# Optimization experiments

Measured on AMD Instinct MI355X. Metric: run time of the kernel, lower is better.

Reference implementation:

```python
import jax, jax.numpy as jnp
import numpy as np

# Directable[TL_table[i]] for i = 0..7: (dx, dy) with dx=horizontal shift, dy=vertical shift
# dx=+1 -> shift right (zero-fill col 0), dx=-1 -> shift left; dy=+1 -> shift down, dy=-1 -> shift up.
DIRS = [(1, 1), (0, 1), (-1, 1), (1, 0), (-1, 0), (1, -1), (0, -1), (-1, -1)]


def _shift(img, dx, dy):
    # img: [B, H, W]; zero-padded shift equivalent to bmm with the sparse translation matrices
    if dx == 1:
        img = jnp.pad(img[..., :-1], ((0, 0), (0, 0), (1, 0)))
    elif dx == -1:
        img = jnp.pad(img[..., 1:], ((0, 0), (0, 0), (0, 1)))
    if dy == 1:
        img = jnp.pad(img[:, :-1, :], ((0, 0), (1, 0), (0, 0)))
    elif dy == -1:
        img = jnp.pad(img[:, 1:, :], ((0, 0), (0, 1), (0, 0)))
    return img


def _bce(p, t):
    # torch F.binary_cross_entropy clamps log terms at -100
    logp = jnp.maximum(jnp.log(p), -100.0)
    log1mp = jnp.maximum(jnp.log(1.0 - p), -100.0)
    return -jnp.mean(t * logp + (1.0 - t) * log1mp)


def setup_inputs() -> dict:
    key = jax.random.key(0)
    k1, k2, k3 = jax.random.split(key, 3)
    B, C, H, W = 16, 8, 512, 512
    c_map = jax.random.normal(k1, (B, C, H, W), dtype=jnp.float32)
    target = jax.random.randint(k2, (B, 1, H, W), 0, 2, dtype=jnp.int32)
    con_target = jax.random.randint(k3, (B, C, H, W), 0, 2, dtype=jnp.int32)
    return {"c_map": c_map, "target": target, "con_target": con_target}


def reference(c_map, target, con_target):
    target = target.astype(jnp.float32)        # [B,1,H,W]
    con_target = con_target.astype(jnp.float32)  # [B,8,H,W]

    p = jax.nn.sigmoid(c_map)  # [B,8,H,W]

    # Bilateral voting: shifted[i] = shift(p[:, 7-i]) in direction DIRS[i]
    shifted = jnp.stack(
        [_shift(p[:, 7 - i], dx, dy) for i, (dx, dy) in enumerate(DIRS)], axis=1
    )  # [B,8,H,W]
    vote_out = p * shifted                       # [B,8,H,W] (== bimap.squeeze(1))
    final_pred = jnp.max(vote_out, axis=1, keepdims=True)  # [B,1,H,W]

    # dice loss (sums over dims (1,2) of the 4D tensors, as in the original)
    smooth = 0.001
    i_sum = jnp.sum(target, axis=(1, 2))
    j_sum = jnp.sum(final_pred, axis=(1, 2))
    inter = jnp.sum(target * final_pred, axis=(1, 2))
    loss_dice = jnp.mean(1.0 - (2.0 * inter + smooth) / (i_sum + j_sum + smooth))

    # edge (decouple) loss
    sum_conn = jnp.sum(con_target, axis=1)  # [B,H,W]
    edge = ((sum_conn < 8) & (sum_conn > 0)).astype(p.dtype)
    pred_min = jnp.min(vote_out, axis=1) * edge
    decouple_loss = _bce(pred_min, jnp.zeros_like(pred_min))

    bce_loss = _bce(final_pred, target)
    conmap_l = _bce(p, con_target)
    bimap_l = _bce(vote_out, con_target)

    return 0.8 * conmap_l + decouple_loss + 0.2 * bimap_l + bce_loss + loss_dice
```

## Files before the change

### kernel.cpp

```cpp
#include <hip/hip_runtime.h>

namespace {
constexpr int Bn = 16, Hn = 512, Wn = 512;
constexpr int HW  = Hn * Wn;
constexpr int CHW = 8 * HW;
constexpr int NCOL = Bn * Wn;
constexpr int WALK = 4;
constexpr int GX   = Hn / WALK;
constexpr int NBLK = GX * Bn;
constexpr int SLABN = NBLK * 512;
constexpr int FBLK  = 32;
constexpr int FBLK2 = 256;

constexpr float L2E  = 1.4426950408889634f;
constexpr float LN2  = 0.6931471805599453f;
constexpr float CLMP = -144.26950408889634f;

__device__ __forceinline__ float frcp(float x) { return __builtin_amdgcn_rcpf(x); }
#if __has_builtin(__builtin_amdgcn_exp2f)
__device__ __forceinline__ float fexp2(float x) { return __builtin_amdgcn_exp2f(x); }
#else
__device__ __forceinline__ float fexp2(float x) { return exp2f(x); }
#endif
#if __has_builtin(__builtin_amdgcn_logf)
__device__ __forceinline__ float flog2(float x) { return __builtin_amdgcn_logf(x); }
#else
__device__ __forceinline__ float flog2(float x) { return log2f(x); }
#endif
}


struct Row {
    float2 a3, a4, a5, a6, a7;
    float2 f0, f1, f2;
    float  b0, b2, b3, b4, b5, b7;
    int2   t;
    int2   u0, u1, u2, u3, u4, u5, u6, u7;
};

template <bool SLAB>
__global__ __launch_bounds__(256) void bicon_main(
    const float* __restrict__ c_map,
    const int*   __restrict__ target,
    const int*   __restrict__ con_target,
    float* __restrict__ col_i, float* __restrict__ col_j, float* __restrict__ col_x,
    double* __restrict__ bscal)
{
    const int tid  = threadIdx.x;
    const int lane = tid & 63;
    const int wv   = tid >> 6;

    const int hwid = blockIdx.y * GX + blockIdx.x;
    const int work = (hwid & 7) * (NBLK / 8) + (hwid >> 3);
    const int gx   = work & (GX - 1);
    const int b    = work >> 7;

    const int hstart = gx * WALK;
    const int wq   = wv * 128 + lane * 2;

    const float* cm = c_map      + (size_t)b * CHW;
    const int*   ct = con_target + (size_t)b * CHW;
    const int*   tg = target     + (size_t)b * HW;

    float s_con = 0.f, s_bi = 0.f, s_bce = 0.f, s_dec = 0.f;
    float ci[2] = {0, 0}, cj[2] = {0, 0}, cx[2] = {0, 0};

    auto sig2 = [&](const float2& v, float s[2]) {
        s[0] = frcp(1.f + fexp2(-v.x * L2E));
        s[1] = frcp(1.f + fexp2(-v.y * L2E));
    };

    auto issue = [&](int hh, Row& R) {
        const int bs = hh * Wn + wq;
        R.a3 = *(const float2*)(cm + 3 * HW + bs);
        R.a4 = *(const float2*)(cm + 4 * HW + bs);
        R.a5 = *(const float2*)(cm + 5 * HW + bs);
        R.a6 = *(const float2*)(cm + 6 * HW + bs);
        R.a7 = *(const float2*)(cm + 7 * HW + bs);
        R.f0 = *(const float2*)(cm + 0 * HW + bs + Wn);
        R.f1 = *(const float2*)(cm + 1 * HW + bs + Wn);
        R.f2 = *(const float2*)(cm + 2 * HW + bs + Wn);
        R.b0 = cm[0 * HW + bs + Wn + 2];
        R.b2 = cm[2 * HW + bs + Wn - 1];
        R.b3 = cm[3 * HW + bs + 2];
        R.b4 = cm[4 * HW + bs - 1];
        R.b5 = cm[5 * HW + bs - Wn + 2];
        R.b7 = cm[7 * HW + bs - Wn - 1];
        R.t  = *(const int2*)(tg + bs);
        R.u0 = *(const int2*)(ct + 0 * HW + bs);
        R.u1 = *(const int2*)(ct + 1 * HW + bs);
        R.u2 = *(const int2*)(ct + 2 * HW + bs);
        R.u3 = *(const int2*)(ct + 3 * HW + bs);
        R.u4 = *(const int2*)(ct + 4 * HW + bs);
        R.u5 = *(const int2*)(ct + 5 * HW + bs);
        R.u6 = *(const int2*)(ct + 6 * HW + bs);
        R.u7 = *(const int2*)(ct + 7 * HW + bs);
    };

    Row cu, nx;
    issue(hstart, cu);

    float C0[2], C1[2], C2[2], P5[2], P6[2], P7[2];
    {
        const int pb = hstart * Wn + wq;
        sig2(*(const float2*)(cm + 0 * HW + pb), C0);
        sig2(*(const float2*)(cm + 1 * HW + pb), C1);
        sig2(*(const float2*)(cm + 2 * HW + pb), C2);
    }
    if (hstart > 0) {
        const int pb = (hstart - 1) * Wn + wq;
        sig2(*(const float2*)(cm + 5 * HW + pb), P5);
        sig2(*(const float2*)(cm + 6 * HW + pb), P6);
        sig2(*(const float2*)(cm + 7 * HW + pb), P7);
    } else {
#pragma unroll
        for (int k = 0; k < 2; ++k) { P5[k] = 0.f; P6[k] = 0.f; P7[k] = 0.f; }
    }

    const bool edR = (wq + 2 == Wn);
    const bool edL = (wq == 0);

#pragma unroll
    for (int r = 0; r < WALK; ++r) {
        const int  h     = hstart + r;
        const int  base  = h * Wn + wq;
        const bool hasDn = (h + 1 < Hn);
        const bool hasUp = (h > 0);

        if (r + 1 < WALK) issue(h + 1, nx);
        (void)base;

        unsigned lo = 0u;
        auto mix = [&](const int2& u, int c) {
            lo |= ((unsigned)u.x << c) | ((unsigned)u.y << (8 + c));
        };
        mix(cu.u0, 0); mix(cu.u1, 1); mix(cu.u2, 2); mix(cu.u3, 3);
        mix(cu.u4, 4); mix(cu.u5, 5); mix(cu.u6, 6); mix(cu.u7, 7);

        float dp[2] = {1.f, 1.f};
        float ys[2] = {0.f, 0.f};
        float c3[2], c4[2], c5[2], c6[2], c7[2];
        auto fresh = [&](int c, const float2& v, float s[2]) {
            const float xs[2] = {v.x, v.y};
#pragma unroll
            for (int k = 0; k < 2; ++k) {
                const float y = xs[k] * L2E;
                const float e = fexp2(-y);
                const float d = 1.f + e;
                s[k] = frcp(d);
                dp[k] *= d;
                ys[k] += ((lo >> (8 * k + c)) & 1u) ? 0.f : y;
            }
        };
        fresh(3, cu.a3, c3); fresh(4, cu.a4, c4); fresh(5, cu.a5, c5);
        fresh(6, cu.a6, c6); fresh(7, cu.a7, c7);

#pragma unroll
        for (int k = 0; k < 2; ++k) {
            const float q0 = ((lo >> (8 * k + 0)) & 1u) ? C0[k] : 1.f - C0[k];
            const float q1 = ((lo >> (8 * k + 1)) & 1u) ? C1[k] : 1.f - C1[k];
            const float q2 = ((lo >> (8 * k + 2)) & 1u) ? C2[k] : 1.f - C2[k];
            s_con += flog2(q0 * q1 * q2) - flog2(dp[k]) - ys[k];
        }

        float F0[2], F1[2], F2[2];
        sig2(cu.f0, F0); sig2(cu.f1, F1); sig2(cu.f2, F2);
        const float s0b = frcp(1.f + fexp2(-cu.b0 * L2E));
        const float s2b = frcp(1.f + fexp2(-cu.b2 * L2E));
        const float s3b = frcp(1.f + fexp2(-cu.b3 * L2E));
        const float s4b = frcp(1.f + fexp2(-cu.b4 * L2E));
        const float s5b = frcp(1.f + fexp2(-cu.b5 * L2E));
        const float s7b = frcp(1.f + fexp2(-cu.b7 * L2E));

        float n0[2], n1[2], n2[2], n3[2], n4[2], n5[2], n6[2], n7[2];
        n0[0] = F0[1]; n3[0] = c3[1]; n5[0] = P5[1];
        n2[1] = F2[0]; n4[1] = c4[0]; n7[1] = P7[0];
        n0[1] = edR ? 0.f : s0b;  n3[1] = edR ? 0.f : s3b;  n5[1] = edR ? 0.f : s5b;
        n2[0] = edL ? 0.f : s2b;  n4[0] = edL ? 0.f : s4b;  n7[0] = edL ? 0.f : s7b;
#pragma unroll
        for (int k = 0; k < 2; ++k) {
            n1[k] = hasDn ? F1[k] : 0.f;
            n6[k] = hasUp ? P6[k] : 0.f;
            if (!hasDn) { n0[k] = 0.f; n2[k] = 0.f; }
            if (!hasUp) { n5[k] = 0.f; n7[k] = 0.f; }
        }

        float vmax[2] = {0.f, 0.f}, vmin[2] = {2.f, 2.f};
        float pr[2]   = {1.f, 1.f};
        float zc[2]   = {0.f, 0.f};
        auto vote = [&](int i, const float p[2], const float n[2]) {
#pragma unroll
            for (int k = 0; k < 2; ++k) {
                const float v = p[k] * n[k];
                vmax[k] = fmaxf(vmax[k], v);
                vmin[k] = fminf(vmin[k], v);
                const bool bit = (lo >> (8 * k + i)) & 1u;
                const bool z   = bit && (v == 0.f);
                float sel = bit ? v : 1.f - v;
                sel = z ? 1.f : sel;
                zc[k] += z ? 1.f : 0.f;
                pr[k] *= sel;
            }
        };
        vote(0, C0, n7); vote(1, C1, n6); vote(2, C2, n5); vote(3, c3, n4);
#pragma unroll
        for (int k = 0; k < 2; ++k) { s_bi += flog2(pr[k]); pr[k] = 1.f; }
        vote(4, c4, n3); vote(5, c5, n2); vote(6, c6, n1); vote(7, c7, n0);
#pragma unroll
        for (int k = 0; k < 2; ++k) { s_bi += flog2(pr[k]) + CLMP * zc[k]; }

        const int tk[2] = {cu.t.x, cu.t.y};
#pragma unroll
        for (int k = 0; k < 2; ++k) {
            const float fm = vmax[k];
            s_bce += fmaxf(flog2(tk[k] ? fm : 1.f - fm), CLMP);
            const int sc = __popc((int)((lo >> (8 * k)) & 0xffu));
            s_dec += (sc > 0 && sc < 8) ? fmaxf(flog2(1.f - vmin[k]), CLMP) : 0.f;
            ci[k] += (float)tk[k];
            cj[k] += fm;
            cx[k] += tk[k] ? fm : 0.f;
        }

#pragma unroll
        for (int k = 0; k < 2; ++k) {
            C0[k] = F0[k]; C1[k] = F1[k]; C2[k] = F2[k];
            P5[k] = c5[k]; P6[k] = c6[k]; P7[k] = c7[k];
        }
        if (r + 1 < WALK) cu = nx;
    }

    if constexpr (SLAB) {
        const size_t sb = ((size_t)work) << 9;
        float2 vi; vi.x = ci[0]; vi.y = ci[1];
        float2 vj; vj.x = cj[0]; vj.y = cj[1];
        float2 vx; vx.x = cx[0]; vx.y = cx[1];
        *(float2*)(col_i + sb + wq) = vi;
        *(float2*)(col_j + sb + wq) = vj;
        *(float2*)(col_x + sb + wq) = vx;
    } else {
#pragma unroll
        for (int k = 0; k < 2; ++k) {
            atomicAdd(&col_i[b * Wn + wq + k], ci[k]);
            atomicAdd(&col_j[b * Wn + wq + k], cj[k]);
            atomicAdd(&col_x[b * Wn + wq + k], cx[k]);
        }
    }

#pragma unroll
    for (int off = 32; off > 0; off >>= 1) {
        s_con += __shfl_down(s_con, off);
        s_bi  += __shfl_down(s_bi,  off);
        s_bce += __shfl_down(s_bce, off);
        s_dec += __shfl_down(s_dec, off);
    }
    __shared__ float wred[4][4];
    if (lane == 0) {
        wred[wv][0] = s_con * LN2; wred[wv][1] = s_bi * LN2;
        wred[wv][2] = s_bce * LN2; wred[wv][3] = s_dec * LN2;
    }
    __syncthreads();
    if (tid < 4) {
        bscal[(size_t)work * 4 + tid] =
            (double)(wred[0][tid] + wred[1][tid] + wred[2][tid] + wred[3][tid]);
    }
}

__global__ __launch_bounds__(256) void bicon_finish_slab(
    const float* __restrict__ pI,
    const float* __restrict__ pJ,
    const float* __restrict__ pX,
    const double* __restrict__ bscal,
    float* __restrict__ out)
{
    const int tid = threadIdx.x;
    const int w32 = tid & 31;
    const int p   = tid >> 5;
    const int col = blockIdx.x * 32 + w32;
    const int b   = col >> 9;
    const int w   = col & 511;

    float fi = 0.f, fj = 0.f, fx = 0.f;
    const size_t base = (((size_t)(b * GX + p * 16)) << 9) + w;
#pragma unroll
    for (int g = 0; g < 16; ++g) {
        const size_t idx = base + ((size_t)g << 9);
        fi += pI[idx]; fj += pJ[idx]; fx += pX[idx];
    }
    __shared__ float red[3][8][32];
    red[0][p][w32] = fi; red[1][p][w32] = fj; red[2][p][w32] = fx;
    __syncthreads();

    double part = 0.0;
    if (tid < 32) {
        float si = 0.f, sj = 0.f, sx = 0.f;
#pragma unroll
        for (int q = 0; q < 8; ++q) {
            si += red[0][q][tid]; sj += red[1][q][tid]; sx += red[2][q][tid];
        }
        part = (1.0 - (2.0 * (double)sx + 0.001) /
                      ((double)si + (double)sj + 0.001)) / 8192.0;
    }
    if (tid >= 64 && tid < 72) {
        const int s = blockIdx.x * 8 + (tid - 64);
        const double c0 = bscal[s * 4 + 0], c1 = bscal[s * 4 + 1];
        const double c2 = bscal[s * 4 + 2], c3 = bscal[s * 4 + 3];
        part += -0.8 * c0 / 33554432.0 - 0.2 * c1 / 33554432.0
                - c2 / 4194304.0 - c3 / 4194304.0;
    }
#pragma unroll
    for (int off = 32; off > 0; off >>= 1) part += __shfl_down(part, off);
    __shared__ double red2[4];
    if ((tid & 63) == 0) red2[tid >> 6] = part;
    __syncthreads();
    if (tid == 0) atomicAdd(out, (float)(red2[0] + red2[1] + red2[2] + red2[3]));
}

__global__ __launch_bounds__(256) void bicon_finish(
    const float* __restrict__ col_i,
    const float* __restrict__ col_j,
    const float* __restrict__ col_x,
    const double* __restrict__ bscal,
    float* __restrict__ out)
{
    const int tid = threadIdx.x;
    const int col = blockIdx.x * 256 + tid;

    double part;
    {
        const float fi = col_i[col], fj = col_j[col], fx = col_x[col];
        part = (1.0 - (2.0 * (double)fx + 0.001) /
                      ((double)fi + (double)fj + 0.001)) / 8192.0;
    }
    if (tid < 64) {
        const int s = blockIdx.x * 64 + tid;
        const double c0 = bscal[s * 4 + 0], c1 = bscal[s * 4 + 1];
        const double c2 = bscal[s * 4 + 2], c3 = bscal[s * 4 + 3];
        part += -0.8 * c0 / 33554432.0 - 0.2 * c1 / 33554432.0
                - c2 / 4194304.0 - c3 / 4194304.0;
    }
#pragma unroll
    for (int off = 32; off > 0; off >>= 1) part += __shfl_down(part, off);
    __shared__ double red[4];
    if ((tid & 63) == 0) red[tid >> 6] = part;
    __syncthreads();
    if (tid == 0) atomicAdd(out, (float)(red[0] + red[1] + red[2] + red[3]));
}

extern "C" void kernel_launch(void* const* d_in, const int* in_sizes, int n_in,
                              void* d_out, int out_size, void* d_ws, size_t ws_size,
                              hipStream_t stream) {
    const float* c_map      = (const float*)d_in[0];
    const int*   target     = (const int*)d_in[1];
    const int*   con_target = (const int*)d_in[2];
    float* out = (float*)d_out;

    char* ws = (char*)d_ws;
    const size_t slab_need = (size_t)3 * SLABN * sizeof(float)
                           + (size_t)NBLK * 4 * sizeof(double);

    dim3 grid(GX, Bn);
    dim3 block(256);

    hipMemsetAsync(d_out, 0, sizeof(float), stream);

    if (ws_size >= slab_need) {
        float*  pI    = (float*)ws;
        float*  pJ    = pI + SLABN;
        float*  pX    = pJ + SLABN;
        double* bscal = (double*)(ws + (size_t)3 * SLABN * sizeof(float));
        bicon_main<true><<<grid, block, 0, stream>>>(c_map, target, con_target,
                                                     pI, pJ, pX, bscal);
        bicon_finish_slab<<<FBLK2, 256, 0, stream>>>(pI, pJ, pX, bscal, out);
    } else {
        float*  col_i = (float*)ws;
        float*  col_j = col_i + NCOL;
        float*  col_x = col_j + NCOL;
        double* bscal = (double*)(ws + 3 * NCOL * sizeof(float));
        hipMemsetAsync(d_ws, 0, 3 * NCOL * sizeof(float), stream);
        bicon_main<false><<<grid, block, 0, stream>>>(c_map, target, con_target,
                                                      col_i, col_j, col_x, bscal);
        bicon_finish<<<FBLK, 256, 0, stream>>>(col_i, col_j, col_x, bscal, out);
    }
}
```

Measured before the change: 299.5 us.

## Double rows per block and share horizontal neighbor sigmoids via wave shuffles

Each block now walks 8 rows instead of 4, which halves the block count and the redundant halo-row loads and sigmoid recomputations. The finish kernels' reduction indexing is adjusted to match. Horizontal neighbour values now come from adjacent lanes through shuffles, so only the edge lanes of each wave issue the scalar halo loads. This cuts scattered loads but gives fewer blocks for latency hiding and adds shuffle instructions.

Result: slower. 333.7 us (+11.4%).

```diff
diff --git a/kernel.cpp b/kernel.cpp
--- a/kernel.cpp
+++ b/kernel.cpp
@@ -5,7 +5,7 @@
 constexpr int HW  = Hn * Wn;
 constexpr int CHW = 8 * HW;
 constexpr int NCOL = Bn * Wn;
-constexpr int WALK = 4;
+constexpr int WALK = 8;
 constexpr int GX   = Hn / WALK;
 constexpr int NBLK = GX * Bn;
 constexpr int SLABN = NBLK * 512;
@@ -53,7 +53,7 @@
     const int hwid = blockIdx.y * GX + blockIdx.x;
     const int work = (hwid & 7) * (NBLK / 8) + (hwid >> 3);
     const int gx   = work & (GX - 1);
-    const int b    = work >> 7;
+    const int b    = work >> 6;
 
     const int hstart = gx * WALK;
     const int wq   = wv * 128 + lane * 2;
@@ -69,6 +69,9 @@
         s[0] = frcp(1.f + fexp2(-v.x * L2E));
         s[1] = frcp(1.f + fexp2(-v.y * L2E));
     };
+
+    const bool lnR = (lane == 63);
+    const bool lnL = (lane == 0);
 
     auto issue = [&](int hh, Row& R) {
         const int bs = hh * Wn + wq;
@@ -80,12 +83,12 @@
         R.f0 = *(const float2*)(cm + 0 * HW + bs + Wn);
         R.f1 = *(const float2*)(cm + 1 * HW + bs + Wn);
         R.f2 = *(const float2*)(cm + 2 * HW + bs + Wn);
-        R.b0 = cm[0 * HW + bs + Wn + 2];
-        R.b2 = cm[2 * HW + bs + Wn - 1];
-        R.b3 = cm[3 * HW + bs + 2];
-        R.b4 = cm[4 * HW + bs - 1];
-        R.b5 = cm[5 * HW + bs - Wn + 2];
-        R.b7 = cm[7 * HW + bs - Wn - 1];
+        R.b0 = lnR ? cm[0 * HW + bs + Wn + 2] : 0.f;
+        R.b3 = lnR ? cm[3 * HW + bs + 2]      : 0.f;
+        R.b5 = lnR ? cm[5 * HW + bs - Wn + 2] : 0.f;
+        R.b2 = lnL ? cm[2 * HW + bs + Wn - 1] : 0.f;
+        R.b4 = lnL ? cm[4 * HW + bs - 1]      : 0.f;
+        R.b7 = lnL ? cm[7 * HW + bs - Wn - 1] : 0.f;
         R.t  = *(const int2*)(tg + bs);
         R.u0 = *(const int2*)(ct + 0 * HW + bs);
         R.u1 = *(const int2*)(ct + 1 * HW + bs);
@@ -123,12 +126,10 @@
 #pragma unroll
     for (int r = 0; r < WALK; ++r) {
         const int  h     = hstart + r;
-        const int  base  = h * Wn + wq;
         const bool hasDn = (h + 1 < Hn);
         const bool hasUp = (h > 0);
 
         if (r + 1 < WALK) issue(h + 1, nx);
-        (void)base;
 
         unsigned lo = 0u;
         auto mix = [&](const int2& u, int c) {
@@ -165,6 +166,13 @@
 
         float F0[2], F1[2], F2[2];
         sig2(cu.f0, F0); sig2(cu.f1, F1); sig2(cu.f2, F2);
+
+        const float r0 = __shfl_down(F0[0], 1);
+        const float r3 = __shfl_down(c3[0], 1);
+        const float r5 = __shfl_down(P5[0], 1);
+        const float l2 = __shfl_up(F2[1], 1);
+        const float l4 = __shfl_up(c4[1], 1);
+        const float l7 = __shfl_up(P7[1], 1);
         const float s0b = frcp(1.f + fexp2(-cu.b0 * L2E));
         const float s2b = frcp(1.f + fexp2(-cu.b2 * L2E));
         const float s3b = frcp(1.f + fexp2(-cu.b3 * L2E));
@@ -175,8 +183,12 @@
         float n0[2], n1[2], n2[2], n3[2], n4[2], n5[2], n6[2], n7[2];
         n0[0] = F0[1]; n3[0] = c3[1]; n5[0] = P5[1];
         n2[1] = F2[0]; n4[1] = c4[0]; n7[1] = P7[0];
-        n0[1] = edR ? 0.f : s0b;  n3[1] = edR ? 0.f : s3b;  n5[1] = edR ? 0.f : s5b;
-        n2[0] = edL ? 0.f : s2b;  n4[0] = edL ? 0.f : s4b;  n7[0] = edL ? 0.f : s7b;
+        n0[1] = edR ? 0.f : (lnR ? s0b : r0);
+        n3[1] = edR ? 0.f : (lnR ? s3b : r3);
+        n5[1] = edR ? 0.f : (lnR ? s5b : r5);
+        n2[0] = edL ? 0.f : (lnL ? s2b : l2);
+        n4[0] = edL ? 0.f : (lnL ? s4b : l4);
+        n7[0] = edL ? 0.f : (lnL ? s7b : l7);
 #pragma unroll
         for (int k = 0; k < 2; ++k) {
             n1[k] = hasDn ? F1[k] : 0.f;
@@ -280,9 +292,9 @@
     const int w   = col & 511;
 
     float fi = 0.f, fj = 0.f, fx = 0.f;
-    const size_t base = (((size_t)(b * GX + p * 16)) << 9) + w;
-#pragma unroll
-    for (int g = 0; g < 16; ++g) {
+    const size_t base = (((size_t)(b * GX + p * 8)) << 9) + w;
+#pragma unroll
+    for (int g = 0; g < 8; ++g) {
         const size_t idx = base + ((size_t)g << 9);
         fi += pI[idx]; fj += pJ[idx]; fx += pX[idx];
     }
@@ -300,8 +312,8 @@
         part = (1.0 - (2.0 * (double)sx + 0.001) /
                       ((double)si + (double)sj + 0.001)) / 8192.0;
     }
-    if (tid >= 64 && tid < 72) {
-        const int s = blockIdx.x * 8 + (tid - 64);
+    if (tid >= 64 && tid < 68) {
+        const int s = blockIdx.x * 4 + (tid - 64);
         const double c0 = bscal[s * 4 + 0], c1 = bscal[s * 4 + 1];
         const double c2 = bscal[s * 4 + 2], c3 = bscal[s * 4 + 3];
         part += -0.8 * c0 / 33554432.0 - 0.2 * c1 / 33554432.0
@@ -331,8 +343,8 @@
         part = (1.0 - (2.0 * (double)fx + 0.001) /
                       ((double)fi + (double)fj + 0.001)) / 8192.0;
     }
-    if (tid < 64) {
-        const int s = blockIdx.x * 64 + tid;
+    if (tid < 32) {
+        const int s = blockIdx.x * 32 + tid;
         const double c0 = bscal[s * 4 + 0], c1 = bscal[s * 4 + 1];
         const double c2 = bscal[s * 4 + 2], c3 = bscal[s * 4 + 3];
         part += -0.8 * c0 / 33554432.0 - 0.2 * c1 / 33554432.0
```
